# Optimization experiments

Measured on AMD Instinct MI355X. Metric: run time of the kernel, lower is better.

## Reference

```python
import jax, jax.numpy as jnp
import numpy as np

E = 1024      # embed_dim
H = 16        # n_heads
B = 8         # number of varlen segments
LQ = 512      # query tokens per segment (uniform packing)
LKV = 1024    # kv tokens per segment (uniform packing)


def setup_inputs() -> dict:
    key = jax.random.key(0)
    k0, k1, k2, k3 = jax.random.split(key, 4)
    inputs = jax.random.normal(k0, (B * LKV, E), dtype=jnp.float32)
    queries = jax.random.normal(k1, (B * LQ, E), dtype=jnp.float32)
    # cu_seqlens: prefix sums of segment lengths (uniform segments here)
    cu_seqlens_inputs = jnp.arange(B + 1, dtype=jnp.int32) * LKV
    cu_seqlens_queries = jnp.arange(B + 1, dtype=jnp.int32) * LQ
    # nn.MultiheadAttention parameters
    scale = 0.02
    w_in = jax.random.normal(k2, (3 * E, E), dtype=jnp.float32) * scale
    b_in = jnp.zeros((3 * E,), dtype=jnp.float32)
    w_out = jax.random.normal(k3, (E, E), dtype=jnp.float32) * scale
    b_out = jnp.zeros((E,), dtype=jnp.float32)
    return {
        "inputs": inputs,
        "queries": queries,
        "w_in": w_in,
        "b_in": b_in,
        "w_out": w_out,
        "b_out": b_out,
        "cu_seqlens_inputs": cu_seqlens_inputs,
        "cu_seqlens_queries": cu_seqlens_queries,
    }


def reference(inputs, queries, w_in, b_in, w_out, b_out,
              cu_seqlens_inputs, cu_seqlens_queries):
    # Packed varlen cross-attention. Segments are uniform (as produced by
    # setup_inputs), so the ragged computation is expressed as a single
    # batched attention: reshape packed tokens to [B, L, E]. Attention is
    # confined within each segment, matching the original per-segment loop.
    e = inputs.shape[-1]
    dh = e // H
    b = cu_seqlens_inputs.shape[0] - 1
    lkv = inputs.shape[0] // b
    lq = queries.shape[0] // b

    # in_proj: torch computes x @ W.T + b with W = in_proj_weight rows [q;k;v]
    q = queries @ w_in[:e].T + b_in[:e]
    k = inputs @ w_in[e:2 * e].T + b_in[e:2 * e]
    v = inputs @ w_in[2 * e:].T + b_in[2 * e:]

    q = q.reshape(b, lq, H, dh)
    k = k.reshape(b, lkv, H, dh)
    v = v.reshape(b, lkv, H, dh)

    scale = 1.0 / jnp.sqrt(jnp.asarray(dh, q.dtype))
    scores = jnp.einsum('bqhd,bkhd->bhqk', q, k) * scale   # [B,H,Lq,Lkv]
    probs = jax.nn.softmax(scores, axis=-1)
    o = jnp.einsum('bhqk,bkhd->bqhd', probs, v).reshape(b * lq, e)
    return o @ w_out.T + b_out
```

## Files before the change

kernel.cpp:

```cpp
#include <hip/hip_runtime.h>

#define E_DIM 1024
#define NH 16
#define DH 64
#define BSEG 8
#define LQ 512
#define LKV 1024

typedef short bf16x8 __attribute__((ext_vector_type(8)));
typedef float f32x4 __attribute__((ext_vector_type(4)));
typedef unsigned short u16;

__device__ __forceinline__ u16 f2bf(float x) {
    unsigned u = __float_as_uint(x);
    u += 0x7FFF + ((u >> 16) & 1);
    return (u16)(u >> 16);
}

__device__ __forceinline__ void async16(const void* g, const void* l) {
    __builtin_amdgcn_global_load_lds(
        (const __attribute__((address_space(1))) unsigned int*)g,
        (__attribute__((address_space(3))) unsigned int*)l, 16, 0, 0);
}

__global__ __launch_bounds__(256) void cvt_all_kernel(
    const float* __restrict__ inputs, const float* __restrict__ queries,
    const float* __restrict__ w_in, const float* __restrict__ w_out,
    u16* __restrict__ ib, u16* __restrict__ qb,
    u16* __restrict__ wib, u16* __restrict__ wob)
{
    int blk = blockIdx.x;
    const float* s; u16* d; int base;
    if (blk < 8192)        { s = inputs;  d = ib;  base = blk; }
    else if (blk < 12288)  { s = queries; d = qb;  base = blk - 8192; }
    else if (blk < 15360)  { s = w_in;    d = wib; base = blk - 12288; }
    else                   { s = w_out;   d = wob; base = blk - 15360; }
    int i = base * 256 + threadIdx.x;
    float4 v = ((const float4*)s)[i];
    ushort4 o;
    o.x = f2bf(v.x); o.y = f2bf(v.y); o.z = f2bf(v.z); o.w = f2bf(v.w);
    ((ushort4*)d)[i] = o;
}

__global__ __launch_bounds__(256) void proj_gemm_kernel(
    const u16* __restrict__ inputs_b, const u16* __restrict__ queries_b,
    const u16* __restrict__ w_in_b, const float* __restrict__ b_in,
    u16* __restrict__ Kf, u16* __restrict__ Qf, u16* __restrict__ Vf)
{
    __shared__ u16 As[128 * 32];
    __shared__ u16 Ws[128 * 32];

    const int bid = blockIdx.x;
    const bool isQ = (bid >= 1024);
    const int x = bid & 7;
    int bx, by;
    if (!isQ) { int i = bid >> 3;          bx = i >> 3; by = x * 8 + (i & 7); }
    else      { int i = (bid - 1024) >> 3; bx = i >> 2; by = x * 4 + (i & 3); }

    const u16* A = isQ ? queries_b : inputs_b;
    const u16* W = w_in_b + (isQ ? 0 : (size_t)E_DIM * E_DIM);
    const float* bias = b_in + (isQ ? 0 : E_DIM);
    const int m_blk = by * 128;
    const int n_blk = bx * 128;
    const int K = E_DIM;

    const int tid = threadIdx.x;
    const int l = tid & 63;
    const int w = tid >> 6;
    const int m0 = (w & 1) * 64;
    const int n0 = (w >> 1) * 64;
    const int quad = l >> 4;
    const int c = l & 15;

    f32x4 acc[4][4];
    #pragma unroll
    for (int i = 0; i < 4; ++i)
        #pragma unroll
        for (int j = 0; j < 4; ++j)
            acc[i][j] = (f32x4){0.f, 0.f, 0.f, 0.f};

    const int srow = l >> 2;
    const int skoff = (l & 3) * 8;
    const u16* Ag1 = A + (size_t)(m_blk + w * 16 + srow) * K + skoff;
    const u16* Ag2 = A + (size_t)(m_blk + (w + 4) * 16 + srow) * K + skoff;
    const u16* Wg1 = W + (size_t)(n_blk + w * 16 + srow) * K + skoff;
    const u16* Wg2 = W + (size_t)(n_blk + (w + 4) * 16 + srow) * K + skoff;

    for (int k0 = 0; k0 < K; k0 += 32) {
        __syncthreads();
        async16(Ag1 + k0, As + (size_t)w * 512);
        async16(Ag2 + k0, As + (size_t)(w + 4) * 512);
        async16(Wg1 + k0, Ws + (size_t)w * 512);
        async16(Wg2 + k0, Ws + (size_t)(w + 4) * 512);
        __syncthreads();

        bf16x8 af[4], wf[4];
        #pragma unroll
        for (int t = 0; t < 4; ++t) {
            af[t] = *(const bf16x8*)&As[(m0 + t * 16 + c) * 32 + quad * 8];
            wf[t] = *(const bf16x8*)&Ws[(n0 + t * 16 + c) * 32 + quad * 8];
        }
        #pragma unroll
        for (int i = 0; i < 4; ++i)
            #pragma unroll
            for (int j = 0; j < 4; ++j)
                acc[i][j] = __builtin_amdgcn_mfma_f32_16x16x32_bf16(
                    af[i], wf[j], acc[i][j], 0, 0, 0);
    }

    #pragma unroll
    for (int jj = 0; jj < 4; ++jj) {
        int col = n_blk + n0 + jj * 16 + c;
        float bv = bias[col];
        if (isQ || col < 1024) {
            u16* dst = isQ ? Qf : Kf;
            int hh = col >> 6, d = col & 63;
            int dq = d >> 3, dj = d & 7;
            #pragma unroll
            for (int i = 0; i < 4; ++i) {
                int t = (m_blk + m0 + i * 16) >> 4;
                size_t base = ((size_t)(t * NH + hh)) * 1024
                            + (size_t)(dq * 16 + quad * 4) * 8 + dj;
                #pragma unroll
                for (int r = 0; r < 4; ++r)
                    dst[base + (size_t)r * 8] = f2bf(acc[i][jj][r] + bv);
            }
        } else {
            int vcol = col - 1024;
            int hv = vcol >> 6, d = vcol & 63;
            int td = d >> 4, ct = d & 15;
            #pragma unroll
            for (int i = 0; i < 4; ++i) {
                int tok = m_blk + m0 + i * 16;
                int g32 = tok >> 5;
                int jo = (tok & 16) >> 2;
                ushort4 pk;
                pk.x = f2bf(acc[i][jj][0] + bv);
                pk.y = f2bf(acc[i][jj][1] + bv);
                pk.z = f2bf(acc[i][jj][2] + bv);
                pk.w = f2bf(acc[i][jj][3] + bv);
                *(ushort4*)(Vf + ((size_t)(g32 * NH + hv)) * 2048
                            + (size_t)((td * 4 + quad) * 16 + ct) * 8 + jo) = pk;
            }
        }
    }
}

struct KVfrags { bf16x8 kf[4][2]; bf16x8 vf[2][4]; };

__global__ __launch_bounds__(256) void attn_kernel(
    const u16* __restrict__ Qf, const u16* __restrict__ Kf,
    const u16* __restrict__ Vf, u16* __restrict__ Ob)
{
    const int tid = threadIdx.x;
    const int l = tid & 63;
    const int w = tid >> 6;
    const int quad = l >> 4;
    const int c = l & 15;
    const int bid = blockIdx.x;
    const int h = bid & 15;
    const int b = (bid >> 4) & 7;
    const int qt = bid >> 7;
    const int q0 = b * LQ + qt * 64 + w * 16;
    const float C1 = 0.18033688011112042f;

    bf16x8 qf[2];
    {
        size_t qb = ((size_t)((q0 >> 4) * NH + h)) * 1024 + (size_t)l * 8;
        qf[0] = *(const bf16x8*)(Qf + qb);
        qf[1] = *(const bf16x8*)(Qf + qb + 512);
    }

    f32x4 o[4];
    #pragma unroll
    for (int td = 0; td < 4; ++td) o[td] = (f32x4){0.f, 0.f, 0.f, 0.f};
    float m_i = -1e30f, l_i = 0.f;

    auto load_kv = [&](int kv0, KVfrags& dst) {
        const int kvg = b * LKV + kv0;
        #pragma unroll
        for (int nt = 0; nt < 4; ++nt) {
            size_t kb = ((size_t)((((kvg >> 4) + nt) * NH) + h)) * 1024 + (size_t)l * 8;
            dst.kf[nt][0] = *(const bf16x8*)(Kf + kb);
            dst.kf[nt][1] = *(const bf16x8*)(Kf + kb + 512);
        }
        #pragma unroll
        for (int g = 0; g < 2; ++g) {
            size_t vb = ((size_t)((((kvg >> 5) + g) * NH) + h)) * 2048 + (size_t)l * 8;
            #pragma unroll
            for (int td = 0; td < 4; ++td)
                dst.vf[g][td] = *(const bf16x8*)(Vf + vb + td * 512);
        }
    };

    auto step = [&](KVfrags& cv) {
        f32x4 s[4];
        #pragma unroll
        for (int nt = 0; nt < 4; ++nt) s[nt] = (f32x4){0.f, 0.f, 0.f, 0.f};
        #pragma unroll
        for (int nt = 0; nt < 4; ++nt)
            #pragma unroll
            for (int hk = 0; hk < 2; ++hk)
                s[nt] = __builtin_amdgcn_mfma_f32_16x16x32_bf16(
                    cv.kf[nt][hk], qf[hk], s[nt], 0, 0, 0);

        float vm = -1e30f;
        #pragma unroll
        for (int nt = 0; nt < 4; ++nt)
            #pragma unroll
            for (int r = 0; r < 4; ++r) vm = fmaxf(vm, s[nt][r]);
        vm = fmaxf(vm, __shfl_xor(vm, 16, 64));
        vm = fmaxf(vm, __shfl_xor(vm, 32, 64));
        float mnew = fmaxf(m_i, vm);
        float alpha = __builtin_amdgcn_exp2f((m_i - mnew) * C1);
        m_i = mnew;

        float p[4][4];
        float rs = 0.f;
        #pragma unroll
        for (int nt = 0; nt < 4; ++nt)
            #pragma unroll
            for (int r = 0; r < 4; ++r) {
                p[nt][r] = __builtin_amdgcn_exp2f((s[nt][r] - mnew) * C1);
                rs += p[nt][r];
            }
        rs += __shfl_xor(rs, 16, 64);
        rs += __shfl_xor(rs, 32, 64);
        l_i = l_i * alpha + rs;

        float ar[4];
        #pragma unroll
        for (int r = 0; r < 4; ++r) ar[r] = __shfl(alpha, quad * 4 + r, 16);
        #pragma unroll
        for (int td = 0; td < 4; ++td)
            #pragma unroll
            for (int r = 0; r < 4; ++r) o[td][r] *= ar[r];

        bf16x8 af[2];
        #pragma unroll
        for (int g = 0; g < 2; ++g)
            #pragma unroll
            for (int r = 0; r < 4; ++r) {
                af[g][r]     = (short)f2bf(p[2 * g][r]);
                af[g][4 + r] = (short)f2bf(p[2 * g + 1][r]);
            }

        #pragma unroll
        for (int g = 0; g < 2; ++g)
            #pragma unroll
            for (int td = 0; td < 4; ++td)
                o[td] = __builtin_amdgcn_mfma_f32_16x16x32_bf16(
                    af[g], cv.vf[g][td], o[td], 0, 0, 0);
    };

    KVfrags bufA, bufB;
    load_kv(0, bufA);
    #pragma unroll
    for (int it = 0; it < 16; it += 2) {
        if (it + 1 < 16) load_kv((it + 1) * 64, bufB);
        step(bufA);
        if (it + 2 < 16) load_kv((it + 2) * 64, bufA);
        if (it + 1 < 16) step(bufB);
    }

    float invl = 1.f / l_i;
    float ir[4];
    #pragma unroll
    for (int r = 0; r < 4; ++r) ir[r] = __shfl(invl, quad * 4 + r, 16);
    #pragma unroll
    for (int td = 0; td < 4; ++td)
        #pragma unroll
        for (int r = 0; r < 4; ++r)
            Ob[(size_t)(q0 + quad * 4 + r) * E_DIM + h * 64 + td * 16 + c] =
                f2bf(o[td][r] * ir[r]);
}

__global__ __launch_bounds__(256) void out_gemm_kernel(
    const u16* __restrict__ A, const u16* __restrict__ W,
    const float* __restrict__ bias, float* __restrict__ Cf)
{
    __shared__ u16 As[128 * 32];
    __shared__ u16 Ws[128 * 32];

    const int K = E_DIM, N = E_DIM;
    const int bid = blockIdx.x;
    const int x = bid & 7;
    const int i_ = bid >> 3;
    const int m_blk = (x * 4 + (i_ & 3)) * 128;
    const int n_blk = (i_ >> 2) * 128;

    const int tid = threadIdx.x;
    const int l = tid & 63;
    const int w = tid >> 6;
    const int m0 = (w & 1) * 64;
    const int n0 = (w >> 1) * 64;
    const int quad = l >> 4;
    const int c = l & 15;

    f32x4 acc[4][4];
    #pragma unroll
    for (int i = 0; i < 4; ++i)
        #pragma unroll
        for (int j = 0; j < 4; ++j)
            acc[i][j] = (f32x4){0.f, 0.f, 0.f, 0.f};

    const int srow = l >> 2;
    const int skoff = (l & 3) * 8;
    const u16* Ag1 = A + (size_t)(m_blk + w * 16 + srow) * K + skoff;
    const u16* Ag2 = A + (size_t)(m_blk + (w + 4) * 16 + srow) * K + skoff;
    const u16* Wg1 = W + (size_t)(n_blk + w * 16 + srow) * K + skoff;
    const u16* Wg2 = W + (size_t)(n_blk + (w + 4) * 16 + srow) * K + skoff;

    for (int k0 = 0; k0 < K; k0 += 32) {
        __syncthreads();
        async16(Ag1 + k0, As + (size_t)w * 512);
        async16(Ag2 + k0, As + (size_t)(w + 4) * 512);
        async16(Wg1 + k0, Ws + (size_t)w * 512);
        async16(Wg2 + k0, Ws + (size_t)(w + 4) * 512);
        __syncthreads();

        bf16x8 af[4], wf[4];
        #pragma unroll
        for (int t = 0; t < 4; ++t) {
            af[t] = *(const bf16x8*)&As[(m0 + t * 16 + c) * 32 + quad * 8];
            wf[t] = *(const bf16x8*)&Ws[(n0 + t * 16 + c) * 32 + quad * 8];
        }
        #pragma unroll
        for (int i = 0; i < 4; ++i)
            #pragma unroll
            for (int j = 0; j < 4; ++j)
                acc[i][j] = __builtin_amdgcn_mfma_f32_16x16x32_bf16(
                    af[i], wf[j], acc[i][j], 0, 0, 0);
    }

    #pragma unroll
    for (int j = 0; j < 4; ++j) {
        int col = n_blk + n0 + j * 16 + c;
        float bv = bias[col];
        #pragma unroll
        for (int i = 0; i < 4; ++i) {
            int row = m_blk + m0 + i * 16 + quad * 4;
            #pragma unroll
            for (int r = 0; r < 4; ++r)
                Cf[(size_t)(row + r) * N + col] = acc[i][j][r] + bv;
        }
    }
}

extern "C" void kernel_launch(void* const* d_in, const int* in_sizes, int n_in,
                              void* d_out, int out_size, void* d_ws, size_t ws_size,
                              hipStream_t stream) {
    const float* inputs  = (const float*)d_in[0];
    const float* queries = (const float*)d_in[1];
    const float* w_in    = (const float*)d_in[2];
    const float* b_in    = (const float*)d_in[3];
    const float* w_out   = (const float*)d_in[4];
    const float* b_out   = (const float*)d_in[5];
    float* out = (float*)d_out;

    const int NQ = BSEG * LQ;
    const int NKV = BSEG * LKV;

    u16* inputs_b  = (u16*)d_ws;
    u16* queries_b = inputs_b  + (size_t)NKV * E_DIM;
    u16* w_in_b    = queries_b + (size_t)NQ * E_DIM;
    u16* w_out_b   = w_in_b    + (size_t)3 * E_DIM * E_DIM;
    u16* Qf        = w_out_b   + (size_t)E_DIM * E_DIM;
    u16* Kf        = Qf        + (size_t)NQ * E_DIM;
    u16* Vf        = Kf        + (size_t)NKV * E_DIM;
    u16* Ob        = Vf        + (size_t)NKV * E_DIM;

    dim3 blk(256);

    cvt_all_kernel<<<16384, blk, 0, stream>>>(
        inputs, queries, w_in, w_out, inputs_b, queries_b, w_in_b, w_out_b);

    proj_gemm_kernel<<<1280, blk, 0, stream>>>(
        inputs_b, queries_b, w_in_b, b_in, Kf, Qf, Vf);

    attn_kernel<<<1024, blk, 0, stream>>>(Qf, Kf, Vf, Ob);

    out_gemm_kernel<<<256, blk, 0, stream>>>(
        Ob, w_out_b, b_out, out);
}
```

Before: 240.8 us.

## Pre-pack operands into MFMA fragment layout and drop LDS staging in GEMMs

```diff
diff --git a/kernel.cpp b/kernel.cpp
--- a/kernel.cpp
+++ b/kernel.cpp
@@ -17,39 +17,39 @@
     return (u16)(u >> 16);
 }
 
-__device__ __forceinline__ void async16(const void* g, const void* l) {
-    __builtin_amdgcn_global_load_lds(
-        (const __attribute__((address_space(1))) unsigned int*)g,
-        (__attribute__((address_space(3))) unsigned int*)l, 16, 0, 0);
-}
 
 __global__ __launch_bounds__(256) void cvt_all_kernel(
     const float* __restrict__ inputs, const float* __restrict__ queries,
     const float* __restrict__ w_in, const float* __restrict__ w_out,
-    u16* __restrict__ ib, u16* __restrict__ qb,
-    u16* __restrict__ wib, u16* __restrict__ wob)
+    u16* __restrict__ ifr, u16* __restrict__ qfr,
+    u16* __restrict__ wifr, u16* __restrict__ wofr)
 {
     int blk = blockIdx.x;
-    const float* s; u16* d; int base;
-    if (blk < 8192)        { s = inputs;  d = ib;  base = blk; }
-    else if (blk < 12288)  { s = queries; d = qb;  base = blk - 8192; }
-    else if (blk < 15360)  { s = w_in;    d = wib; base = blk - 12288; }
-    else                   { s = w_out;   d = wob; base = blk - 15360; }
-    int i = base * 256 + threadIdx.x;
-    float4 v = ((const float4*)s)[i];
-    ushort4 o;
-    o.x = f2bf(v.x); o.y = f2bf(v.y); o.z = f2bf(v.z); o.w = f2bf(v.w);
-    ((ushort4*)d)[i] = o;
+    const float* s; u16* d; int t;
+    if (blk < 512)       { s = inputs;  d = ifr;  t = blk; }
+    else if (blk < 768)  { s = queries; d = qfr;  t = blk - 512; }
+    else if (blk < 960)  { s = w_in;    d = wifr; t = blk - 768; }
+    else                 { s = w_out;   d = wofr; t = blk - 960; }
+    const int tt = threadIdx.x;
+    const int kc = tt >> 4;
+    const int kq = (tt & 15) >> 1;
+    const int jo = (tt & 1) * 4;
+    const float* src = s + (size_t)t * 16 * 1024 + tt * 4;
+    u16* dst = d + ((size_t)t * 16 + kc) * 1024 + kq * 128 + jo;
+    #pragma unroll
+    for (int r = 0; r < 16; ++r) {
+        float4 v = *(const float4*)(src + (size_t)r * 1024);
+        ushort4 o;
+        o.x = f2bf(v.x); o.y = f2bf(v.y); o.z = f2bf(v.z); o.w = f2bf(v.w);
+        *(ushort4*)(dst + r * 8) = o;
+    }
 }
 
 __global__ __launch_bounds__(256) void proj_gemm_kernel(
-    const u16* __restrict__ inputs_b, const u16* __restrict__ queries_b,
-    const u16* __restrict__ w_in_b, const float* __restrict__ b_in,
+    const u16* __restrict__ Afr_in, const u16* __restrict__ Afr_q,
+    const u16* __restrict__ Wfr, const float* __restrict__ b_in,
     u16* __restrict__ Kf, u16* __restrict__ Qf, u16* __restrict__ Vf)
 {
-    __shared__ u16 As[128 * 32];
-    __shared__ u16 Ws[128 * 32];
-
     const int bid = blockIdx.x;
     const bool isQ = (bid >= 1024);
     const int x = bid & 7;
@@ -57,12 +57,11 @@
     if (!isQ) { int i = bid >> 3;          bx = i >> 3; by = x * 8 + (i & 7); }
     else      { int i = (bid - 1024) >> 3; bx = i >> 2; by = x * 4 + (i & 3); }
 
-    const u16* A = isQ ? queries_b : inputs_b;
-    const u16* W = w_in_b + (isQ ? 0 : (size_t)E_DIM * E_DIM);
+    const u16* A = isQ ? Afr_q : Afr_in;
+    const u16* W = Wfr + (isQ ? 0 : (size_t)64 * 16 * 1024);
     const float* bias = b_in + (isQ ? 0 : E_DIM);
     const int m_blk = by * 128;
     const int n_blk = bx * 128;
-    const int K = E_DIM;
 
     const int tid = threadIdx.x;
     const int l = tid & 63;
@@ -72,6 +71,9 @@
     const int quad = l >> 4;
     const int c = l & 15;
 
+    const int tA = (m_blk + m0) >> 4;
+    const int tW = (n_blk + n0) >> 4;
+
     f32x4 acc[4][4];
     #pragma unroll
     for (int i = 0; i < 4; ++i)
@@ -79,33 +81,26 @@
         for (int j = 0; j < 4; ++j)
             acc[i][j] = (f32x4){0.f, 0.f, 0.f, 0.f};
 
-    const int srow = l >> 2;
-    const int skoff = (l & 3) * 8;
-    const u16* Ag1 = A + (size_t)(m_blk + w * 16 + srow) * K + skoff;
-    const u16* Ag2 = A + (size_t)(m_blk + (w + 4) * 16 + srow) * K + skoff;
-    const u16* Wg1 = W + (size_t)(n_blk + w * 16 + srow) * K + skoff;
-    const u16* Wg2 = W + (size_t)(n_blk + (w + 4) * 16 + srow) * K + skoff;
-
-    for (int k0 = 0; k0 < K; k0 += 32) {
-        __syncthreads();
-        async16(Ag1 + k0, As + (size_t)w * 512);
-        async16(Ag2 + k0, As + (size_t)(w + 4) * 512);
-        async16(Wg1 + k0, Ws + (size_t)w * 512);
-        async16(Wg2 + k0, Ws + (size_t)(w + 4) * 512);
-        __syncthreads();
-
-        bf16x8 af[4], wf[4];
-        #pragma unroll
-        for (int t = 0; t < 4; ++t) {
-            af[t] = *(const bf16x8*)&As[(m0 + t * 16 + c) * 32 + quad * 8];
-            wf[t] = *(const bf16x8*)&Ws[(n0 + t * 16 + c) * 32 + quad * 8];
-        }
-        #pragma unroll
-        for (int i = 0; i < 4; ++i)
+    const u16* Ab = A + (size_t)l * 8;
+    const u16* Wb = W + (size_t)l * 8;
+
+    for (int kc = 0; kc < 16; ++kc) {
+        #pragma unroll
+        for (int kh = 0; kh < 2; ++kh) {
+            bf16x8 af[4], wf[4];
+            #pragma unroll
+            for (int i = 0; i < 4; ++i)
+                af[i] = *(const bf16x8*)(Ab + ((size_t)(tA + i) * 16 + kc) * 1024 + kh * 512);
             #pragma unroll
             for (int j = 0; j < 4; ++j)
-                acc[i][j] = __builtin_amdgcn_mfma_f32_16x16x32_bf16(
-                    af[i], wf[j], acc[i][j], 0, 0, 0);
+                wf[j] = *(const bf16x8*)(Wb + ((size_t)(tW + j) * 16 + kc) * 1024 + kh * 512);
+            #pragma unroll
+            for (int i = 0; i < 4; ++i)
+                #pragma unroll
+                for (int j = 0; j < 4; ++j)
+                    acc[i][j] = __builtin_amdgcn_mfma_f32_16x16x32_bf16(
+                        af[i], wf[j], acc[i][j], 0, 0, 0);
+        }
     }
 
     #pragma unroll
@@ -150,7 +145,7 @@
 
 __global__ __launch_bounds__(256) void attn_kernel(
     const u16* __restrict__ Qf, const u16* __restrict__ Kf,
-    const u16* __restrict__ Vf, u16* __restrict__ Ob)
+    const u16* __restrict__ Vf, u16* __restrict__ Obf)
 {
     const int tid = threadIdx.x;
     const int l = tid & 63;
@@ -267,22 +262,22 @@
     float ir[4];
     #pragma unroll
     for (int r = 0; r < 4; ++r) ir[r] = __shfl(invl, quad * 4 + r, 16);
-    #pragma unroll
-    for (int td = 0; td < 4; ++td)
+    size_t obase = ((size_t)((q0 >> 4) * 16 + h)) * 1024;
+    #pragma unroll
+    for (int td = 0; td < 4; ++td) {
+        size_t kpart = (size_t)(td * 2 + (c >> 3)) * 128 + (c & 7);
         #pragma unroll
         for (int r = 0; r < 4; ++r)
-            Ob[(size_t)(q0 + quad * 4 + r) * E_DIM + h * 64 + td * 16 + c] =
+            Obf[obase + kpart + (size_t)(quad * 4 + r) * 8] =
                 f2bf(o[td][r] * ir[r]);
+    }
 }
 
 __global__ __launch_bounds__(256) void out_gemm_kernel(
-    const u16* __restrict__ A, const u16* __restrict__ W,
+    const u16* __restrict__ Afr, const u16* __restrict__ Wfr,
     const float* __restrict__ bias, float* __restrict__ Cf)
 {
-    __shared__ u16 As[128 * 32];
-    __shared__ u16 Ws[128 * 32];
-
-    const int K = E_DIM, N = E_DIM;
+    const int N = E_DIM;
     const int bid = blockIdx.x;
     const int x = bid & 7;
     const int i_ = bid >> 3;
@@ -297,6 +292,9 @@
     const int quad = l >> 4;
     const int c = l & 15;
 
+    const int tA = (m_blk + m0) >> 4;
+    const int tW = (n_blk + n0) >> 4;
+
     f32x4 acc[4][4];
     #pragma unroll
     for (int i = 0; i < 4; ++i)
@@ -304,33 +302,26 @@
         for (int j = 0; j < 4; ++j)
             acc[i][j] = (f32x4){0.f, 0.f, 0.f, 0.f};
 
-    const int srow = l >> 2;
-    const int skoff = (l & 3) * 8;
-    const u16* Ag1 = A + (size_t)(m_blk + w * 16 + srow) * K + skoff;
-    const u16* Ag2 = A + (size_t)(m_blk + (w + 4) * 16 + srow) * K + skoff;
-    const u16* Wg1 = W + (size_t)(n_blk + w * 16 + srow) * K + skoff;
-    const u16* Wg2 = W + (size_t)(n_blk + (w + 4) * 16 + srow) * K + skoff;
-
-    for (int k0 = 0; k0 < K; k0 += 32) {
-        __syncthreads();
-        async16(Ag1 + k0, As + (size_t)w * 512);
-        async16(Ag2 + k0, As + (size_t)(w + 4) * 512);
-        async16(Wg1 + k0, Ws + (size_t)w * 512);
-        async16(Wg2 + k0, Ws + (size_t)(w + 4) * 512);
-        __syncthreads();
-
-        bf16x8 af[4], wf[4];
-        #pragma unroll
-        for (int t = 0; t < 4; ++t) {
-            af[t] = *(const bf16x8*)&As[(m0 + t * 16 + c) * 32 + quad * 8];
-            wf[t] = *(const bf16x8*)&Ws[(n0 + t * 16 + c) * 32 + quad * 8];
-        }
-        #pragma unroll
-        for (int i = 0; i < 4; ++i)
+    const u16* Ab = Afr + (size_t)l * 8;
+    const u16* Wb = Wfr + (size_t)l * 8;
+
+    for (int kc = 0; kc < 16; ++kc) {
+        #pragma unroll
+        for (int kh = 0; kh < 2; ++kh) {
+            bf16x8 af[4], wf[4];
+            #pragma unroll
+            for (int i = 0; i < 4; ++i)
+                af[i] = *(const bf16x8*)(Ab + ((size_t)(tA + i) * 16 + kc) * 1024 + kh * 512);
             #pragma unroll
             for (int j = 0; j < 4; ++j)
-                acc[i][j] = __builtin_amdgcn_mfma_f32_16x16x32_bf16(
-                    af[i], wf[j], acc[i][j], 0, 0, 0);
+                wf[j] = *(const bf16x8*)(Wb + ((size_t)(tW + j) * 16 + kc) * 1024 + kh * 512);
+            #pragma unroll
+            for (int i = 0; i < 4; ++i)
+                #pragma unroll
+                for (int j = 0; j < 4; ++j)
+                    acc[i][j] = __builtin_amdgcn_mfma_f32_16x16x32_bf16(
+                        af[i], wf[j], acc[i][j], 0, 0, 0);
+        }
     }
 
     #pragma unroll
@@ -361,25 +352,25 @@
     const int NQ = BSEG * LQ;
     const int NKV = BSEG * LKV;
 
-    u16* inputs_b  = (u16*)d_ws;
-    u16* queries_b = inputs_b  + (size_t)NKV * E_DIM;
-    u16* w_in_b    = queries_b + (size_t)NQ * E_DIM;
-    u16* w_out_b   = w_in_b    + (size_t)3 * E_DIM * E_DIM;
-    u16* Qf        = w_out_b   + (size_t)E_DIM * E_DIM;
+    u16* inputs_f  = (u16*)d_ws;
+    u16* queries_f = inputs_f  + (size_t)NKV * E_DIM;
+    u16* w_in_f    = queries_f + (size_t)NQ * E_DIM;
+    u16* w_out_f   = w_in_f    + (size_t)3 * E_DIM * E_DIM;
+    u16* Qf        = w_out_f   + (size_t)E_DIM * E_DIM;
     u16* Kf        = Qf        + (size_t)NQ * E_DIM;
     u16* Vf        = Kf        + (size_t)NKV * E_DIM;
-    u16* Ob        = Vf        + (size_t)NKV * E_DIM;
+    u16* Obf       = Vf        + (size_t)NKV * E_DIM;
 
     dim3 blk(256);
 
-    cvt_all_kernel<<<16384, blk, 0, stream>>>(
-        inputs, queries, w_in, w_out, inputs_b, queries_b, w_in_b, w_out_b);
+    cvt_all_kernel<<<1024, blk, 0, stream>>>(
+        inputs, queries, w_in, w_out, inputs_f, queries_f, w_in_f, w_out_f);
 
     proj_gemm_kernel<<<1280, blk, 0, stream>>>(
-        inputs_b, queries_b, w_in_b, b_in, Kf, Qf, Vf);
-
-    attn_kernel<<<1024, blk, 0, stream>>>(Qf, Kf, Vf, Ob);
+        inputs_f, queries_f, w_in_f, b_in, Kf, Qf, Vf);
+
+    attn_kernel<<<1024, blk, 0, stream>>>(Qf, Kf, Vf, Obf);
 
     out_gemm_kernel<<<256, blk, 0, stream>>>(
-        Ob, w_out_b, b_out, out);
-}
+        Obf, w_out_f, b_out, out);
+}
```

After: 252.1 us. 4.7% more time.
